# Optimization experiments

Measured on AMD Instinct MI355X. Metric: run time of the kernel, lower is better.

## Reference

```python
import jax, jax.numpy as jnp
import numpy as np

N = 50000
E = 800000
IN_DIM = 128
HID = 64
HEADS = 4

def _gat_layer(h, src, dst, W, al, ar, Wres, activation):
    # h: [N, F_in]; W: [F_in, HEADS*HID]; al/ar: [HEADS, HID]
    n = h.shape[0]
    ft = (h @ W).reshape(n, HEADS, HID)                    # [N,H,D]
    el = (ft * al).sum(-1)                                  # [N,H]
    er = (ft * ar).sum(-1)                                  # [N,H]
    e = jax.nn.leaky_relu(el[src] + er[dst], 0.2)           # [E,H]
    m = jax.ops.segment_max(e, dst, num_segments=n)         # per-dst max for stable softmax
    ex = jnp.exp(e - m[dst])
    den = jax.ops.segment_sum(ex, dst, num_segments=n)
    alpha = ex / den[dst]                                   # edge softmax [E,H]
    out = jax.ops.segment_sum(alpha[:, :, None] * ft[src], dst, num_segments=n)  # [N,H,D]
    res = (h @ Wres).reshape(n, HEADS, HID) if Wres is not None else h.reshape(n, HEADS, HID)
    out = out + res
    return activation(out) if activation is not None else out


def setup_inputs() -> dict:
    key = jax.random.key(0)
    ks = jax.random.split(key, 16)
    def lin(k, fi, fo):
        return jax.random.normal(k, (fi, fo), jnp.float32) / np.sqrt(fi)
    HD = HEADS * HID
    inp = {
        "h": jax.random.normal(ks[0], (N, IN_DIM), jnp.float32),
        "src": jax.random.randint(ks[1], (E,), 0, N, jnp.int32),
        "dst": jax.random.randint(ks[2], (E,), 0, N, jnp.int32),
        "W1": lin(ks[3], IN_DIM, HD),
        "Wr1": lin(ks[4], IN_DIM, HD),
        "al1": jax.random.normal(ks[5], (HEADS, HID), jnp.float32) * 0.1,
        "ar1": jax.random.normal(ks[6], (HEADS, HID), jnp.float32) * 0.1,
        "W2": lin(ks[7], HD, HD),
        "al2": jax.random.normal(ks[8], (HEADS, HID), jnp.float32) * 0.1,
        "ar2": jax.random.normal(ks[9], (HEADS, HID), jnp.float32) * 0.1,
        "W3": lin(ks[10], HD, HD),
        "al3": jax.random.normal(ks[11], (HEADS, HID), jnp.float32) * 0.1,
        "ar3": jax.random.normal(ks[12], (HEADS, HID), jnp.float32) * 0.1,
        "Wm1": lin(ks[13], HID, HID),
        "bm1": jnp.zeros((HID,), jnp.float32),
        "Wm2": lin(ks[14], HID, 1),
        "bm2": jnp.zeros((1,), jnp.float32),
    }
    return inp


def reference(h, src, dst, W1, Wr1, al1, ar1, W2, al2, ar2, W3, al3, ar3, Wm1, bm1, Wm2, bm2):
    x = _gat_layer(h, src, dst, W1, al1, ar1, Wr1, jax.nn.relu)   # [N,H,D]
    x = x.reshape(x.shape[0], -1)                                  # [N,H*D]
    x = _gat_layer(x, src, dst, W2, al2, ar2, None, jax.nn.relu)  # identity residual (in==H*D)
    x = x.reshape(x.shape[0], -1)
    x = _gat_layer(x, src, dst, W3, al3, ar3, None, None)
    hf = x.mean(1)                                                 # [N,HID]
    diff = jnp.abs(hf[src] - hf[dst])                              # [E,HID]
    z = jax.nn.relu(diff @ Wm1 + bm1)
    score = jax.nn.sigmoid(z @ Wm2 + bm2).squeeze(-1)              # [E]
    return score
```

## Files before the change

### kernel.cpp

```cpp
#include <hip/hip_runtime.h>
#include <hip/hip_bf16.h>

typedef unsigned short u16;
typedef unsigned char u8;
typedef __attribute__((ext_vector_type(8))) short bf16x8;
typedef __attribute__((ext_vector_type(4))) float f32x4;
typedef __attribute__((ext_vector_type(2))) float f32x2;

__device__ __forceinline__ float bf2f(u16 u){
  union { unsigned int i; float f; } v; v.i = ((unsigned int)u) << 16; return v.f;
}
__device__ __forceinline__ u16 f2bf(float f){
  union { float f; unsigned int i; } v; v.f = f;
  unsigned int lsb = (v.i >> 16) & 1u;
  v.i += 0x7fffu + lsb;
  return (u16)(v.i >> 16);
}
__device__ __forceinline__ unsigned pkbf(float a, float b){
  __hip_bfloat162 h = __float22bfloat162_rn(make_float2(a, b));
  union { __hip_bfloat162 h2; unsigned u; } c; c.h2 = h; return c.u;
}
__device__ __forceinline__ u8 f2fp8(float f){
  int p = __builtin_amdgcn_cvt_pk_fp8_f32(f, f, 0, false);
  return (u8)(p & 0xFF);
}

__global__ void k_sniff(const u16* __restrict__ p, int* __restrict__ flag){
  __shared__ int s[256];
  int tid = threadIdx.x;
  u16 v = p[2 * tid];
  int e = (v >> 7) & 0xFF;
  s[tid] = (e >= 100 && e <= 135) ? 1 : 0;
  __syncthreads();
  for (int off = 128; off; off >>= 1){
    if (tid < off) s[tid] += s[tid + off];
    __syncthreads();
  }
  if (tid == 0) *flag = (s[0] < 180) ? 1 : 0;
}

struct PrepEnt { const void* s; void* d; void* d2; int n; int K; int mode; int bstart; };
struct Prep16 { PrepEnt e[16]; };
__global__ void k_prep(Prep16 tab, const u16* __restrict__ hsrc){
  __shared__ int s[256];
  __shared__ u16 tl[32][33];
  {
    int tid = threadIdx.x;
    u16 v = hsrc[2 * tid];
    int e = (v >> 7) & 0xFF;
    s[tid] = (e >= 100 && e <= 135) ? 1 : 0;
    __syncthreads();
    for (int off = 128; off; off >>= 1){
      if (tid < off) s[tid] += s[tid + off];
      __syncthreads();
    }
  }
  const int flag = (s[0] < 180) ? 1 : 0;
  __syncthreads();

  const int bx = blockIdx.x;
  int y = 0;
  #pragma unroll
  for (int i = 1; i < 16; ++i) if (bx >= tab.e[i].bstart) y = i;
  PrepEnt en = tab.e[y];
  const int nblk = ((y < 15) ? tab.e[y + 1].bstart : (int)gridDim.x) - en.bstart;
  const int lb = bx - en.bstart;
  const int T = nblk * 256;
  const int t0 = lb * 256 + threadIdx.x;

  if (en.mode == 1){
    u16* d = (u16*)en.d;
    for (int i = t0; i < en.n; i += T){
      u16 o[4];
      if (flag){
        float4 v = ((const float4*)en.s)[i];
        o[0] = f2bf(v.x); o[1] = f2bf(v.y); o[2] = f2bf(v.z); o[3] = f2bf(v.w);
      } else {
        uint2 v = ((const uint2*)en.s)[i];
        o[0] = (u16)v.x; o[1] = (u16)(v.x >> 16); o[2] = (u16)v.y; o[3] = (u16)(v.y >> 16);
      }
      uint2 w; w.x = o[0] | ((unsigned)o[1] << 16); w.y = o[2] | ((unsigned)o[3] << 16);
      ((uint2*)d)[i] = w;
    }
  } else if (en.mode == 0){
    u16* d = (u16*)en.d;
    for (int i = t0; i < en.n; i += T){
      if (flag) d[i] = f2bf(((const float*)en.s)[i]);
      else      d[i] = ((const u16*)en.s)[i];
    }
  } else if (en.mode == 2){
    u16* wt = (u16*)en.d;
    const int K = en.K;
    const int tk = lb >> 3, tc = lb & 7;
    const int tx = threadIdx.x & 31, ty = threadIdx.x >> 5;
    #pragma unroll
    for (int r = 0; r < 4; ++r){
      int row = tk * 32 + ty + r * 8, col = tc * 32 + tx;
      u16 b;
      if (flag) b = f2bf(((const float*)en.s)[row * 256 + col]);
      else      b = ((const u16*)en.s)[row * 256 + col];
      tl[ty + r * 8][tx] = b;
    }
    __syncthreads();
    #pragma unroll
    for (int r = 0; r < 4; ++r){
      int c = tc * 32 + ty + r * 8, k = tk * 32 + tx;
      wt[(size_t)c * K + k] = tl[tx][ty + r * 8];
    }
  }
}

__global__ void k_scan1(int4* __restrict__ cnt4, int* __restrict__ rowptr,
                        int* __restrict__ bsums, int N){
  __shared__ int s[256];
  int i = blockIdx.x * 256 + threadIdx.x;
  int4 c = make_int4(0, 0, 0, 0);
  if (i < N) c = cnt4[i];
  int v = c.x + c.y + c.z + c.w;
  if (i < N) cnt4[i] = make_int4(0, c.x, c.x + c.y, c.x + c.y + c.z);
  s[threadIdx.x] = v; __syncthreads();
  for (int off = 1; off < 256; off <<= 1){
    int x = 0;
    if (threadIdx.x >= off) x = s[threadIdx.x - off];
    __syncthreads();
    s[threadIdx.x] += x;
    __syncthreads();
  }
  if (i < N) rowptr[i + 1] = s[threadIdx.x];
  if (threadIdx.x == 255) bsums[blockIdx.x] = s[255];
}
__global__ void k_scan2(int* __restrict__ bsums, int nb){
  __shared__ int s[256];
  int t = threadIdx.x;
  int v = (t < nb) ? bsums[t] : 0;
  s[t] = v; __syncthreads();
  for (int off = 1; off < 256; off <<= 1){
    int x = 0;
    if (t >= off) x = s[t - off];
    __syncthreads();
    s[t] += x;
    __syncthreads();
  }
  if (t < nb) bsums[t] = s[t] - v;
}
__global__ void k_scan3(int* __restrict__ rowptr, const int* __restrict__ bsums, int N){
  int i = blockIdx.x * 256 + threadIdx.x;
  if (i < N){
    rowptr[i + 1] += bsums[blockIdx.x];
    if (i == 0) rowptr[0] = 0;
  }
}
__global__ void k_place(const int* __restrict__ src, const int* __restrict__ dst,
                        const int* __restrict__ slot, const int* __restrict__ rowptr,
                        const int* __restrict__ cur4, int4* __restrict__ csrp, int E){
  const int T = gridDim.x * 256;
  for (int i = blockIdx.x * 256 + threadIdx.x; i < E; i += T){
    int d = dst[i];
    int base = cur4[(d << 2) | (i & 3)];
    csrp[rowptr[d] + base + slot[i]] = make_int4(src[i], d, i, 0);
  }
}
__global__ void k_extract(const int4* __restrict__ csrp, int* __restrict__ csrs, int E){
  int i = blockIdx.x * 256 + threadIdx.x;
  if (i < E) csrs[i] = csrp[i].x;
}

__global__ __launch_bounds__(256, 4) void mfma_gemm_v5(
    const u16* __restrict__ X, const u16* __restrict__ WT, const u16* __restrict__ WTr,
    u8* __restrict__ FT8, u16* __restrict__ XA,
    const u16* __restrict__ al, const u16* __restrict__ ar,
    float* __restrict__ el4, float* __restrict__ er4, int N, int K,
    const int* __restrict__ edst, int* __restrict__ slotp, int* __restrict__ cur4,
    int Etot, int do_csr)
{
  extern __shared__ u16 Bs[];
  const int wv = threadIdx.x >> 6;
  const int lane = threadIdx.x & 63;
  const int m = lane & 15;
  const int q = lane >> 4;
  const int row0 = blockIdx.x * 128 + wv * 32;
  const int col0 = blockIdx.y * 128;
  const u16* W = (blockIdx.z == 0) ? WT : WTr;

  {
    const int spr = K >> 3;
    const int ish = (spr == 32) ? 5 : 4;
    const int nIss = K >> 4;
    for (int j = 0; j < nIss; ++j){
      int cbase = (j * 4 + wv) * 64;
      int chunk = cbase + lane;
      int col = chunk >> ish;
      int slot = chunk & (spr - 1);
      int gslot = slot ^ (col & 7);
      const u16* srcp = W + (size_t)(col0 + col) * K + gslot * 8;
      u16* dstp = Bs + (size_t)cbase * 8;
      __builtin_amdgcn_global_load_lds((const unsigned int*)srcp,
                                       (unsigned int*)dstp, 16, 0, 0);
    }
  }

  f32x4 acc[2][8];
  #pragma unroll
  for (int g = 0; g < 2; ++g)
    #pragma unroll
    for (int t = 0; t < 8; ++t) acc[g][t] = (f32x4){0.f, 0.f, 0.f, 0.f};
  const int rA = row0 + m, rB = row0 + 16 + m;
  const bool vA = rA < N, vB = rB < N;
  const u16* apA = X + (size_t)rA * K + q * 8;
  const u16* apB = X + (size_t)rB * K + q * 8;

  asm volatile("s_waitcnt vmcnt(0)" ::: "memory");
  __syncthreads();

  const int mh = m & 7;
  for (int k0 = 0; k0 < K; k0 += 32){
    bf16x8 aA = {}, aB = {};
    if (vA) aA = *(const bf16x8*)(apA + k0);
    if (vB) aB = *(const bf16x8*)(apB + k0);
    const int sb = (k0 >> 3) + q;
    #pragma unroll
    for (int t = 0; t < 8; ++t){
      const u16* bp = Bs + (size_t)(t * 16 + m) * K + (size_t)(sb ^ mh) * 8;
      bf16x8 b = *(const bf16x8*)bp;
      acc[0][t] = __builtin_amdgcn_mfma_f32_16x16x32_bf16(aA, b, acc[0][t], 0, 0, 0);
      acc[1][t] = __builtin_amdgcn_mfma_f32_16x16x32_bf16(aB, b, acc[1][t], 0, 0, 0);
    }
  }

  int ce0 = 0, ce1 = 0, cp0 = 0, cp1 = 0;
  bool cb0 = false, cb1 = false;
  if (do_csr){
    const int nbk = gridDim.x * 4;
    const int bid = ((blockIdx.z * 2 + blockIdx.y) * gridDim.x) + blockIdx.x;
    const int epb = (Etot + nbk - 1) / nbk;
    const int elo = bid * epb;
    const int ehi = min(elo + epb, Etot);
    ce0 = elo + (int)threadIdx.x;
    ce1 = ce0 + 256;
    cb0 = ce0 < ehi; cb1 = ce1 < ehi;
    int d0 = 0, d1 = 0;
    if (cb0) d0 = edst[ce0];
    if (cb1) d1 = edst[ce1];
    if (cb0) cp0 = atomicAdd(&cur4[(d0 << 2) | (ce0 & 3)], 1);
    if (cb1) cp1 = atomicAdd(&cur4[(d1 << 2) | (ce1 & 3)], 1);
    for (int e = elo + (int)threadIdx.x + 512; e < ehi; e += 256){
      int dd = edst[e];
      slotp[e] = atomicAdd(&cur4[(dd << 2) | (e & 3)], 1);
    }
  }

  if (blockIdx.z == 0){
    float alv[8], arv[8];
    #pragma unroll
    for (int t = 0; t < 8; ++t){
      alv[t] = bf2f(al[col0 + t * 16 + m]);
      arv[t] = bf2f(ar[col0 + t * 16 + m]);
    }
    #pragma unroll
    for (int g = 0; g < 2; ++g)
      #pragma unroll
      for (int r = 0; r < 4; ++r){
        float pe[2] = {0.f, 0.f}, pr[2] = {0.f, 0.f};
        #pragma unroll
        for (int t = 0; t < 8; ++t){
          pe[t >> 2] += acc[g][t][r] * alv[t];
          pr[t >> 2] += acc[g][t][r] * arv[t];
        }
        #pragma unroll
        for (int mk = 1; mk < 16; mk <<= 1){
          pe[0] += __shfl_xor(pe[0], mk); pe[1] += __shfl_xor(pe[1], mk);
          pr[0] += __shfl_xor(pr[0], mk); pr[1] += __shfl_xor(pr[1], mk);
        }
        int rr = row0 + g * 16 + q * 4 + r;
        if (m == 0 && rr < N){
          *(float2*)(el4 + (size_t)rr * 4 + blockIdx.y * 2) = make_float2(pe[0], pe[1]);
          *(float2*)(er4 + (size_t)rr * 4 + blockIdx.y * 2) = make_float2(pr[0], pr[1]);
        }
      }
    #pragma unroll
    for (int g = 0; g < 2; ++g)
      #pragma unroll
      for (int t = 0; t < 8; ++t){
        int col = col0 + t * 16 + m;
        #pragma unroll
        for (int r = 0; r < 4; ++r){
          int rr = row0 + g * 16 + q * 4 + r;
          if (rr < N) FT8[(size_t)rr * 256 + col] = f2fp8(acc[g][t][r]);
        }
      }
  } else {
    #pragma unroll
    for (int g = 0; g < 2; ++g)
      #pragma unroll
      for (int t = 0; t < 8; ++t){
        int col = col0 + t * 16 + m;
        #pragma unroll
        for (int r = 0; r < 4; ++r){
          int rr = row0 + g * 16 + q * 4 + r;
          if (rr < N) XA[(size_t)rr * 256 + col] = f2bf(acc[g][t][r]);
        }
      }
  }

  if (do_csr){
    if (cb0) slotp[ce0] = cp0;
    if (cb1) slotp[ce1] = cp1;
  }
}

__global__ __launch_bounds__(256) void aggregate8(
    const u8* __restrict__ ft8, const float* __restrict__ el4, const float* __restrict__ er4,
    const int* __restrict__ rowptr, const int* __restrict__ csrs,
    const u16* __restrict__ residb, u16* __restrict__ outb,
    u16* __restrict__ hf, int do_hf, int N)
{
  __shared__ float sal[4][4][17][4];
  __shared__ int   sof[4][4][16];
  const int w = threadIdx.x >> 6, lane = threadIdx.x & 63;
  const int g = lane >> 4, t = lane & 15;
  const int hd = t >> 2;
  const int d = blockIdx.x * 16 + w * 4 + g;
  const bool vd = d < N;
  int beg = 0, deg = 0;
  if (vd){ beg = rowptr[d]; deg = rowptr[d + 1] - beg; }
  int mdeg = deg;
  mdeg = max(mdeg, __shfl_xor(mdeg, 16));
  mdeg = max(mdeg, __shfl_xor(mdeg, 32));
  float4 erd = make_float4(0.f, 0.f, 0.f, 0.f);
  if (vd) erd = ((const float4*)er4)[d];

  f32x2 acc2[8];
  #pragma unroll
  for (int i = 0; i < 8; ++i) acc2[i] = (f32x2){0.f, 0.f};
  float den[4] = {0.f, 0.f, 0.f, 0.f};

  for (int c0 = 0; c0 < mdeg; c0 += 16){
    const int rem = deg - c0;
    float t0 = 0.f, t1 = 0.f, t2 = 0.f, t3 = 0.f; int s = 0;
    if (t < rem){
      s = csrs[beg + c0 + t];
      float4 ql = ((const float4*)el4)[s];
      float e0 = ql.x + erd.x; e0 = (e0 > 0.f) ? e0 : 0.2f * e0;
      float e1 = ql.y + erd.y; e1 = (e1 > 0.f) ? e1 : 0.2f * e1;
      float e2 = ql.z + erd.z; e2 = (e2 > 0.f) ? e2 : 0.2f * e2;
      float e3 = ql.w + erd.w; e3 = (e3 > 0.f) ? e3 : 0.2f * e3;
      t0 = __expf(fminf(e0, 60.f)); t1 = __expf(fminf(e1, 60.f));
      t2 = __expf(fminf(e2, 60.f)); t3 = __expf(fminf(e3, 60.f));
    }
    den[0] += t0; den[1] += t1; den[2] += t2; den[3] += t3;
    sal[w][g][t][0] = t0; sal[w][g][t][1] = t1;
    sal[w][g][t][2] = t2; sal[w][g][t][3] = t3;
    sof[w][g][t] = s << 8;
    __builtin_amdgcn_wave_barrier();
    int cr = rem < 16 ? (rem < 0 ? 0 : rem) : 16;
    int jm = (cr + 3) & ~3;
    for (int j = 0; j < jm; j += 4){
      float a[4]; unsigned off[4]; uint4 v[4];
      #pragma unroll
      for (int u = 0; u < 4; ++u){
        a[u] = sal[w][g][j + u][hd];
        off[u] = (unsigned)sof[w][g][j + u];
      }
      #pragma unroll
      for (int u = 0; u < 4; ++u)
        v[u] = *(const uint4*)(ft8 + (size_t)off[u] + t * 16);
      #pragma unroll
      for (int u = 0; u < 4; ++u){
        f32x2 a2 = (f32x2){a[u], a[u]};
        acc2[0] += __builtin_amdgcn_cvt_pk_f32_fp8(v[u].x, 0) * a2;
        acc2[1] += __builtin_amdgcn_cvt_pk_f32_fp8(v[u].x, 1) * a2;
        acc2[2] += __builtin_amdgcn_cvt_pk_f32_fp8(v[u].y, 0) * a2;
        acc2[3] += __builtin_amdgcn_cvt_pk_f32_fp8(v[u].y, 1) * a2;
        acc2[4] += __builtin_amdgcn_cvt_pk_f32_fp8(v[u].z, 0) * a2;
        acc2[5] += __builtin_amdgcn_cvt_pk_f32_fp8(v[u].z, 1) * a2;
        acc2[6] += __builtin_amdgcn_cvt_pk_f32_fp8(v[u].w, 0) * a2;
        acc2[7] += __builtin_amdgcn_cvt_pk_f32_fp8(v[u].w, 1) * a2;
      }
    }
    __builtin_amdgcn_wave_barrier();
  }
  #pragma unroll
  for (int mk = 1; mk < 16; mk <<= 1){
    den[0] += __shfl_xor(den[0], mk); den[1] += __shfl_xor(den[1], mk);
    den[2] += __shfl_xor(den[2], mk); den[3] += __shfl_xor(den[3], mk);
  }
  const float dh = den[hd];
  const float inv = (dh > 0.f) ? (1.f / dh) : 0.f;

  if (!vd) return;
  const u16* rp = residb + (size_t)d * 256 + t * 16;
  uint4 r0 = *(const uint4*)rp;
  uint4 r1 = *(const uint4*)(rp + 8);
  float o[16];
  {
    union { unsigned u; float f; } x;
    unsigned rw[8] = {r0.x, r0.y, r0.z, r0.w, r1.x, r1.y, r1.z, r1.w};
    #pragma unroll
    for (int i = 0; i < 8; ++i){
      x.u = rw[i] << 16;          o[2 * i]     = x.f;
      x.u = rw[i] & 0xffff0000u;  o[2 * i + 1] = x.f;
    }
  }
  #pragma unroll
  for (int i = 0; i < 8; ++i){
    o[2 * i]     += acc2[i].x * inv;
    o[2 * i + 1] += acc2[i].y * inv;
  }
  if (!do_hf){
    uint4 a, b;
    a.x = pkbf(fmaxf(o[0], 0.f),  fmaxf(o[1], 0.f));
    a.y = pkbf(fmaxf(o[2], 0.f),  fmaxf(o[3], 0.f));
    a.z = pkbf(fmaxf(o[4], 0.f),  fmaxf(o[5], 0.f));
    a.w = pkbf(fmaxf(o[6], 0.f),  fmaxf(o[7], 0.f));
    b.x = pkbf(fmaxf(o[8], 0.f),  fmaxf(o[9], 0.f));
    b.y = pkbf(fmaxf(o[10], 0.f), fmaxf(o[11], 0.f));
    b.z = pkbf(fmaxf(o[12], 0.f), fmaxf(o[13], 0.f));
    b.w = pkbf(fmaxf(o[14], 0.f), fmaxf(o[15], 0.f));
    u16* op = outb + (size_t)d * 256 + t * 16;
    *(uint4*)op = a;
    *(uint4*)(op + 8) = b;
  } else {
    #pragma unroll
    for (int i = 0; i < 16; ++i){
      float v = o[i];
      v += __shfl_xor(v, 4);
      v += __shfl_xor(v, 8);
      o[i] = 0.25f * v;
    }
    if (t < 4){
      uint4 a, b;
      a.x = pkbf(o[0], o[1]);   a.y = pkbf(o[2], o[3]);
      a.z = pkbf(o[4], o[5]);   a.w = pkbf(o[6], o[7]);
      b.x = pkbf(o[8], o[9]);   b.y = pkbf(o[10], o[11]);
      b.z = pkbf(o[12], o[13]); b.w = pkbf(o[14], o[15]);
      u16* hp = hf + (size_t)d * 64 + t * 16;
      *(uint4*)hp = a;
      *(uint4*)(hp + 8) = b;
    }
  }
}

__global__ __launch_bounds__(256) void edge_mlp_csr(
    const u16* __restrict__ hfb, const int4* __restrict__ csrp,
    const u16* __restrict__ Wm1, const u16* __restrict__ bm1,
    const u16* __restrict__ Wm2, const u16* __restrict__ bm2,
    void* __restrict__ out, int E, const int* __restrict__ flag)
{
  const int lane = threadIdx.x & 63;
  const int m = lane & 15;
  const int q = lane >> 4;
  const int is_f32 = *flag;

  bf16x8 bfr[4][2];
  #pragma unroll
  for (int t = 0; t < 4; ++t)
    #pragma unroll
    for (int ks = 0; ks < 2; ++ks)
      #pragma unroll
      for (int j = 0; j < 8; ++j)
        bfr[t][ks][j] = (short)Wm1[(size_t)(ks * 32 + q * 8 + j) * 64 + t * 16 + m];

  float b1v[4], w2v[4];
  #pragma unroll
  for (int t = 0; t < 4; ++t){
    b1v[t] = bf2f(bm1[t * 16 + m]);
    w2v[t] = bf2f(Wm2[t * 16 + m]);
  }
  const float b2 = bf2f(bm2[0]);

  const int wid = blockIdx.x * 4 + (threadIdx.x >> 6);
  const int nw  = gridDim.x * 4;
  for (int e0 = wid * 16; e0 < E; e0 += nw * 16){
    int e = e0 + m; if (e >= E) e = E - 1;
    int4 ed = csrp[e];
    const u16* ps = hfb + (size_t)ed.x * 64;
    const u16* pd = hfb + (size_t)ed.y * 64;
    union { bf16x8 v; uint4 u; } af[2];
    #pragma unroll
    for (int ks = 0; ks < 2; ++ks){
      bf16x8 vs = *(const bf16x8*)(ps + ks * 32 + q * 8);
      bf16x8 vd = *(const bf16x8*)(pd + ks * 32 + q * 8);
      unsigned pk[4];
      #pragma unroll
      for (int pp = 0; pp < 4; ++pp){
        float a0 = fabsf(bf2f((u16)vs[2 * pp])     - bf2f((u16)vd[2 * pp]));
        float a1 = fabsf(bf2f((u16)vs[2 * pp + 1]) - bf2f((u16)vd[2 * pp + 1]));
        pk[pp] = pkbf(a0, a1);
      }
      af[ks].u = make_uint4(pk[0], pk[1], pk[2], pk[3]);
    }
    f32x4 acc[4];
    #pragma unroll
    for (int t = 0; t < 4; ++t) acc[t] = (f32x4){0.f, 0.f, 0.f, 0.f};
    #pragma unroll
    for (int ks = 0; ks < 2; ++ks)
      #pragma unroll
      for (int t = 0; t < 4; ++t)
        acc[t] = __builtin_amdgcn_mfma_f32_16x16x32_bf16(af[ks].v, bfr[t][ks], acc[t], 0, 0, 0);
    #pragma unroll
    for (int r = 0; r < 4; ++r){
      float p = 0.f;
      #pragma unroll
      for (int t = 0; t < 4; ++t)
        p += fmaxf(acc[t][r] + b1v[t], 0.f) * w2v[t];
      #pragma unroll
      for (int mm = 1; mm < 16; mm <<= 1) p += __shfl_xor(p, mm);
      int slot = e0 + q * 4 + r;
      if (m == 0 && slot < E){
        int eid = csrp[slot].z;
        float sc = 1.f / (1.f + __expf(-(p + b2)));
        if (is_f32) ((float*)out)[eid] = sc;
        else        ((u16*)out)[eid]   = f2bf(sc);
      }
    }
  }
}

extern "C" void kernel_launch(void* const* d_in, const int* in_sizes, int n_in,
                              void* d_out, int out_size, void* d_ws, size_t ws_size,
                              hipStream_t stream)
{
  const int* src = (const int*)d_in[1];
  const int* dst = (const int*)d_in[2];

  const int N = in_sizes[0] / 128;
  const int E = in_sizes[1];

  char* p = (char*)d_ws;
  auto alloc = [&](size_t bytes) -> char* {
    char* r = p; p += (bytes + 255) & ~(size_t)255; return r;
  };
  int* flag   = (int*)  alloc(4);
  u16* hc     = (u16*)  alloc((size_t)N * 128 * 2);
  u8*  FT8    = (u8*)   alloc((size_t)N * 256);
  u16* XA     = (u16*)  alloc((size_t)N * 256 * 2);
  u16* XB     = (u16*)  alloc((size_t)N * 256 * 2);
  float* el   = (float*)alloc((size_t)N * 4 * 4);
  float* er   = (float*)alloc((size_t)N * 4 * 4);
  u16* hfb    = (u16*)  alloc((size_t)N * 64 * 2);
  int* rowptr = (int*)  alloc((size_t)(N + 1) * 4);
  int* cur4   = (int*)  alloc((size_t)N * 16);
  int* slot   = (int*)  alloc((size_t)E * 4);
  int4* csrp  = (int4*) alloc((size_t)E * 16);
  int* csrs   = (int*)  alloc((size_t)E * 4);
  int* bsums  = (int*)  alloc(1024);
  u16* WT1    = (u16*)  alloc(128 * 256 * 2);
  u16* WTr1   = (u16*)  alloc(128 * 256 * 2);
  u16* WT2    = (u16*)  alloc(256 * 256 * 2);
  u16* WT3    = (u16*)  alloc(256 * 256 * 2);
  u16* al1c   = (u16*)  alloc(256 * 2);
  u16* ar1c   = (u16*)  alloc(256 * 2);
  u16* al2c   = (u16*)  alloc(256 * 2);
  u16* ar2c   = (u16*)  alloc(256 * 2);
  u16* al3c   = (u16*)  alloc(256 * 2);
  u16* ar3c   = (u16*)  alloc(256 * 2);
  u16* Wm1c   = (u16*)  alloc(4096 * 2);
  u16* bm1c   = (u16*)  alloc(64 * 2);
  u16* Wm2c   = (u16*)  alloc(64 * 2);
  u16* bm2c   = (u16*)  alloc(2);

  const int nb = (N + 255) / 256;
  const int ge = (E + 255) / 256;
  const u16* hsrc = (const u16*)d_in[0];

  k_sniff<<<1, 256, 0, stream>>>(hsrc, flag);
  hipMemsetAsync(cur4, 0, (size_t)N * 16, stream);

  {
    Prep16 t{};
    int b = 0;
    auto put = [&](int idx, const void* s, void* d, void* d2, int n, int K,
                   int mode, int nblk){
      t.e[idx] = {s, d, d2, n, K, mode, b};
      b += nblk;
    };
    put(0,  d_in[0],  hc,    nullptr, N * 32,   0,   1, 768);
    put(1,  d_in[3],  WT1,   nullptr, 0,        128, 2, 32);
    put(2,  d_in[4],  WTr1,  nullptr, 0,        128, 2, 32);
    put(3,  d_in[7],  WT2,   nullptr, 0,        256, 2, 64);
    put(4,  d_in[10], WT3,   nullptr, 0,        256, 2, 64);
    put(5,  d_in[5],  al1c,  nullptr, 256,      0,   0, 1);
    put(6,  d_in[6],  ar1c,  nullptr, 256,      0,   0, 1);
    put(7,  d_in[8],  al2c,  nullptr, 256,      0,   0, 1);
    put(8,  d_in[9],  ar2c,  nullptr, 256,      0,   0, 1);
    put(9,  d_in[11], al3c,  nullptr, 256,      0,   0, 1);
    put(10, d_in[12], ar3c,  nullptr, 256,      0,   0, 1);
    put(11, d_in[13], Wm1c,  nullptr, 4096,     0,   0, 1);
    put(12, d_in[14], bm1c,  nullptr, 64,       0,   0, 1);
    put(13, d_in[15], Wm2c,  nullptr, 64,       0,   0, 1);
    put(14, d_in[16], bm2c,  nullptr, 1,        0,   0, 1);
    put(15, nullptr,  nullptr, nullptr, 0,      0,   0, 0);
    k_prep<<<dim3(b), 256, 0, stream>>>(t, hsrc);
  }

  const dim3 gA3((N + 127) / 128, 2);
  const dim3 gL1((N + 127) / 128, 2, 2);
  const int gG = (N + 15) / 16;
  const int lds1 = 128 * 128 * 2;
  const int lds2 = 128 * 256 * 2;

  mfma_gemm_v5<<<gL1, 256, lds1, stream>>>(hc, WT1, WTr1, FT8, XA, al1c, ar1c,
                                           el, er, N, 128, dst, slot, cur4, E, 1);
  k_scan1<<<nb, 256, 0, stream>>>((int4*)cur4, rowptr, bsums, N);
  k_scan2<<<1, 256, 0, stream>>>(bsums, nb);
  k_scan3<<<nb, 256, 0, stream>>>(rowptr, bsums, N);
  k_place<<<512, 256, 0, stream>>>(src, dst, slot, rowptr, cur4, csrp, E);
  k_extract<<<ge, 256, 0, stream>>>(csrp, csrs, E);

  aggregate8<<<gG, 256, 0, stream>>>(FT8, el, er, rowptr, csrs, XA, XB, nullptr, 0, N);
  mfma_gemm_v5<<<gA3, 256, lds2, stream>>>(XB, WT2, WT2, FT8, XA, al2c, ar2c,
                                           el, er, N, 256, nullptr, nullptr, nullptr, 0, 0);
  aggregate8<<<gG, 256, 0, stream>>>(FT8, el, er, rowptr, csrs, XB, XA, nullptr, 0, N);
  mfma_gemm_v5<<<gA3, 256, lds2, stream>>>(XA, WT3, WT3, FT8, XB, al3c, ar3c,
                                           el, er, N, 256, nullptr, nullptr, nullptr, 0, 0);
  aggregate8<<<gG, 256, 0, stream>>>(FT8, el, er, rowptr, csrs, XA, nullptr, hfb, 1, N);
  edge_mlp_csr<<<2048, 256, 0, stream>>>(hfb, csrp, Wm1c, bm1c, Wm2c, bm2c,
                                         d_out, E, flag);
}
```

Baseline: 397.6 us.

## Double-buffer GEMM weight tiles in LDS with K-chunked async staging

The GEMM no longer loads the whole weight panel into LDS before computing. It now streams 64-wide K chunks into two LDS buffers and prefetches the next chunk of weights and A fragments while the current one is computed. This shrinks LDS per block (32KB instead of 64KB for K=256), which can allow more resident blocks, and hides load latency behind MFMA work. The cost is extra barriers and partial vmcnt waits, and the vmcnt(8) count has to match the number of outstanding loads issued per stage.

New measurement: 401.9 us. Within noise of the previous version (+1.1%).

```diff
diff --git a/kernel.cpp b/kernel.cpp
--- a/kernel.cpp
+++ b/kernel.cpp
@@ -165,7 +165,11 @@
   if (i < E) csrs[i] = csrp[i].x;
 }
 
-__global__ __launch_bounds__(256, 4) void mfma_gemm_v5(
+#define GWAIT8() asm volatile("s_waitcnt vmcnt(8)" ::: "memory")
+#define GWAIT0() asm volatile("s_waitcnt vmcnt(0)" ::: "memory")
+#define GBAR()   do { __builtin_amdgcn_s_barrier(); __builtin_amdgcn_sched_barrier(0); } while (0)
+
+__global__ __launch_bounds__(256, 4) void mfma_gemm_v6(
     const u16* __restrict__ X, const u16* __restrict__ WT, const u16* __restrict__ WTr,
     u8* __restrict__ FT8, u16* __restrict__ XA,
     const u16* __restrict__ al, const u16* __restrict__ ar,
@@ -178,26 +182,10 @@
   const int lane = threadIdx.x & 63;
   const int m = lane & 15;
   const int q = lane >> 4;
+  const int mh = m & 7;
   const int row0 = blockIdx.x * 128 + wv * 32;
   const int col0 = blockIdx.y * 128;
   const u16* W = (blockIdx.z == 0) ? WT : WTr;
-
-  {
-    const int spr = K >> 3;
-    const int ish = (spr == 32) ? 5 : 4;
-    const int nIss = K >> 4;
-    for (int j = 0; j < nIss; ++j){
-      int cbase = (j * 4 + wv) * 64;
-      int chunk = cbase + lane;
-      int col = chunk >> ish;
-      int slot = chunk & (spr - 1);
-      int gslot = slot ^ (col & 7);
-      const u16* srcp = W + (size_t)(col0 + col) * K + gslot * 8;
-      u16* dstp = Bs + (size_t)cbase * 8;
-      __builtin_amdgcn_global_load_lds((const unsigned int*)srcp,
-                                       (unsigned int*)dstp, 16, 0, 0);
-    }
-  }
 
   f32x4 acc[2][8];
   #pragma unroll
@@ -209,21 +197,57 @@
   const u16* apA = X + (size_t)rA * K + q * 8;
   const u16* apB = X + (size_t)rB * K + q * 8;
 
-  asm volatile("s_waitcnt vmcnt(0)" ::: "memory");
-  __syncthreads();
-
-  const int mh = m & 7;
-  for (int k0 = 0; k0 < K; k0 += 32){
-    bf16x8 aA = {}, aB = {};
-    if (vA) aA = *(const bf16x8*)(apA + k0);
-    if (vB) aB = *(const bf16x8*)(apB + k0);
-    const int sb = (k0 >> 3) + q;
-    #pragma unroll
-    for (int t = 0; t < 8; ++t){
-      const u16* bp = Bs + (size_t)(t * 16 + m) * K + (size_t)(sb ^ mh) * 8;
-      bf16x8 b = *(const bf16x8*)bp;
-      acc[0][t] = __builtin_amdgcn_mfma_f32_16x16x32_bf16(aA, b, acc[0][t], 0, 0, 0);
-      acc[1][t] = __builtin_amdgcn_mfma_f32_16x16x32_bf16(aB, b, acc[1][t], 0, 0, 0);
+  auto stageC = [&](int c, int buf){
+    u16* base = Bs + buf * 8192;
+    const u16* Wk = W + c * 64;
+    #pragma unroll
+    for (int j = 0; j < 4; ++j){
+      int cbase = (j * 4 + wv) * 64;
+      int ci = cbase + lane;
+      int col = ci >> 3, slot = ci & 7;
+      int gslot = slot ^ (col & 7);
+      const u16* srcp = Wk + (size_t)(col0 + col) * K + gslot * 8;
+      __builtin_amdgcn_global_load_lds((const unsigned int*)srcp,
+                                       (unsigned int*)(base + cbase * 8), 16, 0, 0);
+    }
+  };
+  auto loadA = [&](int c, bf16x8* a){
+    const int kb = c * 64;
+    bf16x8 z = {};
+    a[0] = z; a[1] = z; a[2] = z; a[3] = z;
+    if (vA){ a[0] = *(const bf16x8*)(apA + kb); a[2] = *(const bf16x8*)(apA + kb + 32); }
+    if (vB){ a[1] = *(const bf16x8*)(apB + kb); a[3] = *(const bf16x8*)(apB + kb + 32); }
+  };
+  auto compute = [&](const u16* __restrict__ Bb, const bf16x8* a){
+    #pragma unroll
+    for (int ks = 0; ks < 2; ++ks){
+      const int sb = ks * 4 + q;
+      #pragma unroll
+      for (int t = 0; t < 8; ++t){
+        const u16* bp = Bb + (size_t)(t * 16 + m) * 64 + (size_t)(sb ^ mh) * 8;
+        bf16x8 b = *(const bf16x8*)bp;
+        acc[0][t] = __builtin_amdgcn_mfma_f32_16x16x32_bf16(a[2 * ks],     b, acc[0][t], 0, 0, 0);
+        acc[1][t] = __builtin_amdgcn_mfma_f32_16x16x32_bf16(a[2 * ks + 1], b, acc[1][t], 0, 0, 0);
+      }
+    }
+  };
+
+  const int nc = K >> 6;
+  bf16x8 a0[4], a1[4];
+  stageC(0, 0);
+  loadA(0, a0);
+  for (int c = 0; c < nc; c += 2){
+    if (c + 1 < nc){ stageC(c + 1, 1); loadA(c + 1, a1); GWAIT8(); }
+    else           { GWAIT0(); }
+    GBAR();
+    compute(Bs, a0);
+    GBAR();
+    if (c + 1 < nc){
+      if (c + 2 < nc){ stageC(c + 2, 0); loadA(c + 2, a0); GWAIT8(); }
+      else           { GWAIT0(); }
+      GBAR();
+      compute(Bs + 8192, a1);
+      GBAR();
     }
   }
 
@@ -596,10 +620,9 @@
   const dim3 gA3((N + 127) / 128, 2);
   const dim3 gL1((N + 127) / 128, 2, 2);
   const int gG = (N + 15) / 16;
-  const int lds1 = 128 * 128 * 2;
-  const int lds2 = 128 * 256 * 2;
-
-  mfma_gemm_v5<<<gL1, 256, lds1, stream>>>(hc, WT1, WTr1, FT8, XA, al1c, ar1c,
+  const int ldsP = 2 * 128 * 64 * 2;
+
+  mfma_gemm_v6<<<gL1, 256, ldsP, stream>>>(hc, WT1, WTr1, FT8, XA, al1c, ar1c,
                                            el, er, N, 128, dst, slot, cur4, E, 1);
   k_scan1<<<nb, 256, 0, stream>>>((int4*)cur4, rowptr, bsums, N);
   k_scan2<<<1, 256, 0, stream>>>(bsums, nb);
@@ -608,10 +631,10 @@
   k_extract<<<ge, 256, 0, stream>>>(csrp, csrs, E);
 
   aggregate8<<<gG, 256, 0, stream>>>(FT8, el, er, rowptr, csrs, XA, XB, nullptr, 0, N);
-  mfma_gemm_v5<<<gA3, 256, lds2, stream>>>(XB, WT2, WT2, FT8, XA, al2c, ar2c,
+  mfma_gemm_v6<<<gA3, 256, ldsP, stream>>>(XB, WT2, WT2, FT8, XA, al2c, ar2c,
                                            el, er, N, 256, nullptr, nullptr, nullptr, 0, 0);
   aggregate8<<<gG, 256, 0, stream>>>(FT8, el, er, rowptr, csrs, XB, XA, nullptr, 0, N);
-  mfma_gemm_v5<<<gA3, 256, lds2, stream>>>(XA, WT3, WT3, FT8, XB, al3c, ar3c,
+  mfma_gemm_v6<<<gA3, 256, ldsP, stream>>>(XA, WT3, WT3, FT8, XB, al3c, ar3c,
                                            el, er, N, 256, nullptr, nullptr, nullptr, 0, 0);
   aggregate8<<<gG, 256, 0, stream>>>(FT8, el, er, rowptr, csrs, XA, nullptr, hfb, 1, N);
   edge_mlp_csr<<<2048, 256, 0, stream>>>(hfb, csrp, Wm1c, bm1c, Wm2c, bm2c,
```
